# Kernel tuning notes

Hardware: AMD Instinct MI355X
Metric: run time of the kernel (lower is better)

Reference implementation:

```python
import jax, jax.numpy as jnp
import numpy as np

D = 512      # encoder_dim
DI = 1024    # mamba d_inner = expand * d_model
N = 16       # d_state
DTR = 32     # dt_rank = ceil(512/16)
K = 4        # d_conv
B, L = 8, 512


def _ln(x, g, b, eps=1e-5):
    m = jnp.mean(x, -1, keepdims=True)
    v = jnp.mean((x - m) ** 2, -1, keepdims=True)
    return (x - m) / jnp.sqrt(v + eps) * g + b


def _silu(x):
    return x * jax.nn.sigmoid(x)


def _ffn(x, g, b, w1, b1, w2, b2):
    h = _ln(x, g, b)
    h = _silu(h @ w1.T + b1)
    return h @ w2.T + b2


def _dwconv(x, w, pl, pr):
    # x: (B,C,L); w: (C,K) depthwise kernel
    return jax.lax.conv_general_dilated(
        x, w[:, None, :], (1,), [(pl, pr)],
        feature_group_count=x.shape[1], dimension_numbers=('NCH', 'OIH', 'NCH'))


def _mamba(x, win, convw, convb, wx, wdt, bdt, Alog, Dp, wout):
    b = x.shape[0]
    xz = jnp.einsum('bld,ed->ble', x, win)            # (B,L,2*DI)
    xi, z = jnp.split(xz, 2, -1)
    xc = _dwconv(xi.transpose(0, 2, 1), convw, K - 1, 0) + convb[None, :, None]
    xc = _silu(xc).transpose(0, 2, 1)                 # (B,L,DI) causal conv + silu
    xdb = jnp.einsum('bld,ed->ble', xc, wx)           # (B,L,DTR+2N)
    dt, Bm, Cm = xdb[..., :DTR], xdb[..., DTR:DTR + N], xdb[..., DTR + N:]
    dt = jax.nn.softplus(jnp.einsum('blr,dr->bld', dt, wdt) + bdt)
    A = -jnp.exp(Alog)                                # (DI,N)
    dA = jnp.exp(dt[..., None] * A)                   # (B,L,DI,N)
    dBx = dt[..., None] * Bm[:, :, None, :] * xc[..., None]

    def step(h, t):
        dA_t, dBx_t, C_t = t
        h = dA_t * h + dBx_t
        return h, jnp.einsum('bdn,bn->bd', h, C_t)

    h0 = jnp.zeros((b, DI, N), x.dtype)
    _, ys = jax.lax.scan(step, h0, (dA.transpose(1, 0, 2, 3),
                                    dBx.transpose(1, 0, 2, 3),
                                    Cm.transpose(1, 0, 2)))
    y = ys.transpose(1, 0, 2) + Dp * xc
    y = y * _silu(z)
    return jnp.einsum('bld,od->blo', y, wout)


def _bimamba(x, m_win, m_convw, m_convb, m_wx, m_wdt, m_bdt, m_Alog, m_D, m_wout, bi_wo, bi_bo):
    f = _mamba(x, m_win[0], m_convw[0], m_convb[0], m_wx[0], m_wdt[0], m_bdt[0],
               m_Alog[0], m_D[0], m_wout[0])
    r = _mamba(x[:, ::-1], m_win[1], m_convw[1], m_convb[1], m_wx[1], m_wdt[1], m_bdt[1],
               m_Alog[1], m_D[1], m_wout[1])
    cat = jnp.concatenate([f, r[:, ::-1]], -1)
    return cat @ bi_wo.T + bi_bo


def _convmod(x, ln_g, ln_b, pw1_w, pw1_b, dw15, dw31, dw63,
             bn_g, bn_b, bn_m, bn_v, pw2_w, pw2_b):
    h = _ln(x, ln_g, ln_b).transpose(0, 2, 1)          # (B,D,L)
    h = jnp.einsum('bcl,oc->bol', h, pw1_w) + pw1_b[None, :, None]
    a, g = jnp.split(h, 2, 1)
    h = a * jax.nn.sigmoid(g)                          # GLU on channel dim
    outs = [_dwconv(h, w, (w.shape[-1] - 1) // 2, (w.shape[-1] - 1) // 2)
            for w in (dw15, dw31, dw63)]
    out = (outs[0] + outs[1] + outs[2]) / 3.0          # merge_mode='avg'
    out = (out - bn_m[None, :, None]) / jnp.sqrt(bn_v[None, :, None] + 1e-5) \
          * bn_g[None, :, None] + bn_b[None, :, None]
    out = _silu(out)
    out = jnp.einsum('bcl,oc->bol', out, pw2_w) + pw2_b[None, :, None]
    return out.transpose(0, 2, 1)


def setup_inputs() -> dict:
    key = jax.random.key(0)
    ks = iter(jax.random.split(key, 64))
    def w(*shape, s=0.02):
        return jax.random.normal(next(ks), shape, jnp.float32) * s
    inp = {}
    inp['x'] = jax.random.normal(next(ks), (B, L, D), jnp.float32)
    for p in ('ff1', 'ff2'):
        inp[p + '_ln_g'] = jnp.ones((D,), jnp.float32)
        inp[p + '_ln_b'] = jnp.zeros((D,), jnp.float32)
        inp[p + '_w1'] = w(4 * D, D)
        inp[p + '_b1'] = jnp.zeros((4 * D,), jnp.float32)
        inp[p + '_w2'] = w(D, 4 * D)
        inp[p + '_b2'] = jnp.zeros((D,), jnp.float32)
    inp['m_win'] = w(2, 2 * DI, D)
    inp['m_convw'] = w(2, DI, K, s=0.1)
    inp['m_convb'] = jnp.zeros((2, DI), jnp.float32)
    inp['m_wx'] = w(2, DTR + 2 * N, DI)
    inp['m_wdt'] = w(2, DI, DTR, s=0.1)
    inp['m_bdt'] = jnp.full((2, DI), float(np.log(np.expm1(0.01))), jnp.float32)
    inp['m_Alog'] = jnp.log(jnp.tile(jnp.arange(1, N + 1, dtype=jnp.float32), (2, DI, 1)))
    inp['m_D'] = jnp.ones((2, DI), jnp.float32)
    inp['m_wout'] = w(2, D, DI)
    inp['bi_wo'] = w(D, 2 * D)
    inp['bi_bo'] = jnp.zeros((D,), jnp.float32)
    inp['cv_ln_g'] = jnp.ones((D,), jnp.float32)
    inp['cv_ln_b'] = jnp.zeros((D,), jnp.float32)
    inp['cv_pw1_w'] = w(2 * D, D)
    inp['cv_pw1_b'] = jnp.zeros((2 * D,), jnp.float32)
    inp['cv_dw15'] = w(D, 15, s=0.1)
    inp['cv_dw31'] = w(D, 31, s=0.1)
    inp['cv_dw63'] = w(D, 63, s=0.1)
    inp['cv_bn_g'] = jnp.ones((D,), jnp.float32)
    inp['cv_bn_b'] = jnp.zeros((D,), jnp.float32)
    inp['cv_bn_m'] = jnp.zeros((D,), jnp.float32)
    inp['cv_bn_v'] = jnp.ones((D,), jnp.float32)
    inp['cv_pw2_w'] = w(D, D)
    inp['cv_pw2_b'] = jnp.zeros((D,), jnp.float32)
    inp['ln_g'] = jnp.ones((D,), jnp.float32)
    inp['ln_b'] = jnp.zeros((D,), jnp.float32)
    return inp


def reference(x, ff1_ln_g, ff1_ln_b, ff1_w1, ff1_b1, ff1_w2, ff1_b2,
              ff2_ln_g, ff2_ln_b, ff2_w1, ff2_b1, ff2_w2, ff2_b2,
              m_win, m_convw, m_convb, m_wx, m_wdt, m_bdt, m_Alog, m_D, m_wout,
              bi_wo, bi_bo,
              cv_ln_g, cv_ln_b, cv_pw1_w, cv_pw1_b, cv_dw15, cv_dw31, cv_dw63,
              cv_bn_g, cv_bn_b, cv_bn_m, cv_bn_v, cv_pw2_w, cv_pw2_b,
              ln_g, ln_b):
    h = x + 0.5 * _ffn(x, ff1_ln_g, ff1_ln_b, ff1_w1, ff1_b1, ff1_w2, ff1_b2)
    h = h + _bimamba(h, m_win, m_convw, m_convb, m_wx, m_wdt, m_bdt,
                     m_Alog, m_D, m_wout, bi_wo, bi_bo)
    h = h + _convmod(h, cv_ln_g, cv_ln_b, cv_pw1_w, cv_pw1_b, cv_dw15, cv_dw31, cv_dw63,
                     cv_bn_g, cv_bn_b, cv_bn_m, cv_bn_v, cv_pw2_w, cv_pw2_b)
    h = h + 0.5 * _ffn(h, ff2_ln_g, ff2_ln_b, ff2_w1, ff2_b1, ff2_w2, ff2_b2)
    return _ln(h, ln_g, ln_b)
```

## Files before the change

kernel.cpp:

```cpp
#include <hip/hip_runtime.h>
#include <hip/hip_bf16.h>
#include <math.h>

#define LL   512
#define DD   512
#define DII  1024
#define NST  16
#define BB   8
#define MM   4096
#define CHL  32
#define NCH  16
#define MB_  (1024*1024)
#define Q_(n) ((size_t)(n)*262144)

typedef __attribute__((ext_vector_type(8))) short bf16x8;
typedef __attribute__((ext_vector_type(4))) float f32x4;

__device__ __forceinline__ float fast_rcp(float x){ return __builtin_amdgcn_rcpf(x); }
__device__ __forceinline__ float sigmoidf_(float x){ return fast_rcp(1.0f + __expf(-x)); }
__device__ __forceinline__ float siluf_(float x){ return x * sigmoidf_(x); }
__device__ __forceinline__ float softplusf_(float x){
    return fmaxf(x, 0.0f) + __logf(1.0f + __expf(-fabsf(x)));
}

__device__ __forceinline__ short f2bf(float f) {
    union { float f; unsigned u; } v; v.f = f;
    unsigned r = v.u + 0x7fffu + ((v.u >> 16) & 1u);
    return (short)(r >> 16);
}
__device__ __forceinline__ float bf2f(short s) {
    union { unsigned u; float f; } v; v.u = ((unsigned)(unsigned short)s) << 16;
    return v.f;
}
__device__ __forceinline__ bf16x8 pack_bf8(float4 v0, float4 v1) {
    union { bf16x8 v; short e[8]; } pk;
    pk.e[0]=f2bf(v0.x); pk.e[1]=f2bf(v0.y); pk.e[2]=f2bf(v0.z); pk.e[3]=f2bf(v0.w);
    pk.e[4]=f2bf(v1.x); pk.e[5]=f2bf(v1.y); pk.e[6]=f2bf(v1.z); pk.e[7]=f2bf(v1.w);
    return pk.v;
}
__device__ __forceinline__ void gl_lds16(const short* g, short* l) {
    __builtin_amdgcn_global_load_lds(
        (const __attribute__((address_space(1))) void*)g,
        (__attribute__((address_space(3))) void*)l, 16, 0, 0);
}

struct WcvtArgs { const float* s[10]; short* d[10]; int n[10]; };
__global__ void __launch_bounds__(256) wcvt_kernel(WcvtArgs a) {
    const int seg = blockIdx.y;
    const int i = (blockIdx.x*256 + threadIdx.x) * 8;
    if (i >= a.n[seg]) return;
    const float* s = a.s[seg] + i;
    float4 v0 = *(const float4*)s;
    float4 v1 = *(const float4*)(s + 4);
    int di = i;
    if (seg == 8) di = ((i >> 5) << 6) | (i & 31);
    *(bf16x8*)(a.d[seg] + di) = pack_bf8(v0, v1);
}

__global__ void __launch_bounds__(256) woutT_kernel(
    const float* __restrict__ wout, short* __restrict__ outT)
{
    __shared__ float sh[64][65];
    const int o0 = blockIdx.x << 6;
    const int j0 = blockIdx.y << 6;
    const int d  = blockIdx.z;
    const float* in = wout + (size_t)d*512*1024;
    short* out = outT + (size_t)d*1024*512;
    const int t = threadIdx.x;
    const int c4 = (t & 15) << 2;
    const int r  = t >> 4;
    #pragma unroll
    for (int i = 0; i < 4; i++) {
        int orow = r + i*16;
        float4 v = *(const float4*)(in + (size_t)(o0 + orow)*1024 + j0 + c4);
        sh[orow][c4+0]=v.x; sh[orow][c4+1]=v.y; sh[orow][c4+2]=v.z; sh[orow][c4+3]=v.w;
    }
    __syncthreads();
    #pragma unroll
    for (int i = 0; i < 4; i++) {
        int jr = r + i*16;
        short4 o;
        o.x = f2bf(sh[c4+0][jr]); o.y = f2bf(sh[c4+1][jr]);
        o.z = f2bf(sh[c4+2][jr]); o.w = f2bf(sh[c4+3][jr]);
        *(short4*)(out + (size_t)(j0 + jr)*512 + o0 + c4) = o;
    }
}

template<int BN>
__global__ void __launch_bounds__(256) gemm3_kernel(
    const short* __restrict__ A, int lda,
    const short* __restrict__ W, int ldw,
    const float* __restrict__ bias,
    float* __restrict__ outF, short* __restrict__ outB, int ldc,
    int kLen, int kOff, int act, int actLim,
    size_t zA, size_t zW, int zB, size_t zO, int rowsPerW,
    float* __restrict__ partial, size_t pstride, int N)
{
    constexpr int WN = BN / 64;
    constexpr int WM = 4 / WN;
    constexpr int TM = 64 / WM;
    constexpr int FM = TM / 16;
    constexpr int WRW = BN / 32;

    __shared__ short As[2][64*64];
    __shared__ short Ws[2][BN*64];

    const int tid = threadIdx.x, lane = tid & 63, wid = tid >> 6;
    const int z = blockIdx.z;
    A += (size_t)z * zA;
    if (outF) outF += (size_t)z * zO;
    if (outB) outB += (size_t)z * zO;

    int nwg = gridDim.x * gridDim.y;
    int flat = blockIdx.y * gridDim.x + blockIdx.x;
    if (!(nwg & 7)) { int cpx = nwg >> 3; flat = (flat & 7)*cpx + (flat >> 3); }
    const int bx = flat % gridDim.x, by = flat / gridDim.x;

    const int rowBase = by << 6;
    const int colBase = bx * BN;
    const int kBase = z * kOff;

    const int dsel = rowsPerW ? (rowBase / rowsPerW) : z;
    W += (size_t)dsel * zW;
    if (bias) bias += (size_t)dsel * (size_t)zB;

    size_t asrc[2];
    #pragma unroll
    for (int rd = 0; rd < 2; rd++) {
        int id = rd*256 + tid, row = id >> 3, u = id & 7;
        asrc[rd] = (size_t)(rowBase + row)*lda + ((u ^ (row & 7)) << 3);
    }
    size_t wsrc[WRW];
    #pragma unroll
    for (int rd = 0; rd < WRW; rd++) {
        int id = rd*256 + tid, row = id >> 3, u = id & 7;
        wsrc[rd] = (size_t)(colBase + row)*ldw + ((u ^ (row & 7)) << 3);
    }

    const int fr = lane & 15;
    const int swz0 = ((((lane >> 4)    ) ^ (lane & 7)) << 3);
    const int swz1 = ((((lane >> 4) | 4) ^ (lane & 7)) << 3);
    const int wm = (wid / WN) * TM, wn = (wid % WN) * 64;

    f32x4 acc[FM][4] = {};

    auto STAGE = [&](int buf, int k0) {
        #pragma unroll
        for (int rd = 0; rd < 2; rd++)
            gl_lds16(A + asrc[rd] + k0, &As[buf][(rd*256 + tid)*8]);
        #pragma unroll
        for (int rd = 0; rd < WRW; rd++)
            gl_lds16(W + wsrc[rd] + k0, &Ws[buf][(rd*256 + tid)*8]);
    };

    const int nT = kLen >> 6;
    STAGE(0, kBase);
    int cur = 0;
    for (int t = 0; t < nT; ++t) {
        if (t + 1 < nT) {
            STAGE(cur ^ 1, kBase + (t+1)*64);
            asm volatile("s_waitcnt vmcnt(6)" ::: "memory");
        } else {
            asm volatile("s_waitcnt vmcnt(0)" ::: "memory");
        }
        __builtin_amdgcn_sched_barrier(0);
        __builtin_amdgcn_s_barrier();
        __builtin_amdgcn_sched_barrier(0);
        #pragma unroll
        for (int ks = 0; ks < 2; ks++) {
            const int so = ks ? swz1 : swz0;
            bf16x8 af[FM], bfr[4];
            #pragma unroll
            for (int mi = 0; mi < FM; mi++)
                af[mi] = *(const bf16x8*)&As[cur][(wm + mi*16 + fr)*64 + so];
            #pragma unroll
            for (int ni = 0; ni < 4; ni++)
                bfr[ni] = *(const bf16x8*)&Ws[cur][(wn + ni*16 + fr)*64 + so];
            #pragma unroll
            for (int mi = 0; mi < FM; mi++)
                #pragma unroll
                for (int ni = 0; ni < 4; ni++)
                    acc[mi][ni] = __builtin_amdgcn_mfma_f32_16x16x32_bf16(af[mi], bfr[ni], acc[mi][ni], 0, 0, 0);
        }
        __builtin_amdgcn_sched_barrier(0);
        __builtin_amdgcn_s_barrier();
        __builtin_amdgcn_sched_barrier(0);
        cur ^= 1;
    }

    if (partial) {
        float* pp = partial + (size_t)z * pstride;
        #pragma unroll
        for (int mi = 0; mi < FM; mi++)
            #pragma unroll
            for (int r = 0; r < 4; r++) {
                int orow = rowBase + wm + mi*16 + ((lane>>4)<<2) + r;
                #pragma unroll
                for (int ni = 0; ni < 4; ni++)
                    pp[(size_t)orow*N + colBase + wn + ni*16 + fr] = acc[mi][ni][r];
            }
    } else {
        #pragma unroll
        for (int mi = 0; mi < FM; mi++)
            #pragma unroll
            for (int r = 0; r < 4; r++) {
                int orow = rowBase + wm + mi*16 + ((lane>>4)<<2) + r;
                #pragma unroll
                for (int ni = 0; ni < 4; ni++) {
                    int gcol = colBase + wn + ni*16 + fr;
                    float v = acc[mi][ni][r];
                    if (bias) v += bias[gcol];
                    if (gcol < actLim) {
                        if (act == 1) v = siluf_(v);
                        else if (act == 2) v = softplusf_(v);
                    }
                    if (outF) outF[(size_t)orow*ldc + gcol] = v;
                    if (outB) outB[(size_t)orow*ldc + gcol] = f2bf(v);
                }
            }
    }
}

__global__ void __launch_bounds__(256) reduce_kernel(
    const float* __restrict__ part, int S, size_t pstride, int N,
    short* __restrict__ outB, int ldc)
{
    const int i4 = blockIdx.x*256 + threadIdx.x;
    const int row = i4 / (N >> 2);
    const int c4  = (i4 - row*(N >> 2)) << 2;
    float4 s = *(const float4*)(part + (size_t)row*N + c4);
    for (int z = 1; z < S; z++) {
        float4 t = *(const float4*)(part + (size_t)z*pstride + (size_t)row*N + c4);
        s.x += t.x; s.y += t.y; s.z += t.z; s.w += t.w;
    }
    short4 o; o.x=f2bf(s.x); o.y=f2bf(s.y); o.z=f2bf(s.z); o.w=f2bf(s.w);
    *(short4*)(outB + (size_t)row*ldc + c4) = o;
}

__global__ void __launch_bounds__(128) redln_kernel(
    const float* __restrict__ part, int S,
    const float* __restrict__ bias,
    const float* __restrict__ resid, float rscale,
    float* __restrict__ houtF, short* __restrict__ houtB,
    const float* __restrict__ lng, const float* __restrict__ lnb2,
    float* __restrict__ lnoutF, short* __restrict__ lnoutB)
{
    const int row = blockIdx.x;
    const int t = threadIdx.x;
    const size_t pstride = (size_t)MM*512;
    float4 s = ((const float4*)(part + (size_t)row*512))[t];
    for (int z = 1; z < S; z++) {
        float4 v = ((const float4*)(part + z*pstride + (size_t)row*512))[t];
        s.x += v.x; s.y += v.y; s.z += v.z; s.w += v.w;
    }
    if (bias) { float4 b = ((const float4*)bias)[t]; s.x+=b.x; s.y+=b.y; s.z+=b.z; s.w+=b.w; }
    if (resid) {
        float4 r = ((const float4*)(resid + (size_t)row*512))[t];
        s.x = r.x + rscale*s.x; s.y = r.y + rscale*s.y;
        s.z = r.z + rscale*s.z; s.w = r.w + rscale*s.w;
    }
    if (houtF) ((float4*)(houtF + (size_t)row*512))[t] = s;
    if (houtB) {
        short4 o; o.x=f2bf(s.x); o.y=f2bf(s.y); o.z=f2bf(s.z); o.w=f2bf(s.w);
        *(short4*)(houtB + (size_t)row*512 + t*4) = o;
    }
    if (!lng) return;
    float sum = s.x+s.y+s.z+s.w;
    float sq  = s.x*s.x+s.y*s.y+s.z*s.z+s.w*s.w;
    #pragma unroll
    for (int off = 32; off >= 1; off >>= 1) {
        sum += __shfl_down(sum, off);
        sq  += __shfl_down(sq, off);
    }
    __shared__ float sh[4];
    if ((t & 63) == 0) { sh[(t>>6)*2] = sum; sh[(t>>6)*2+1] = sq; }
    __syncthreads();
    float mean = (sh[0]+sh[2]) * (1.0f/512.f);
    float var  = (sh[1]+sh[3]) * (1.0f/512.f) - mean*mean;
    float rstd = rsqrtf(var + 1e-5f);
    float4 gg = ((const float4*)lng)[t];
    float4 bb = ((const float4*)lnb2)[t];
    float4 o;
    o.x = (s.x-mean)*rstd*gg.x + bb.x;
    o.y = (s.y-mean)*rstd*gg.y + bb.y;
    o.z = (s.z-mean)*rstd*gg.z + bb.z;
    o.w = (s.w-mean)*rstd*gg.w + bb.w;
    if (lnoutF) ((float4*)(lnoutF + (size_t)row*512))[t] = o;
    if (lnoutB) {
        short4 ob; ob.x=f2bf(o.x); ob.y=f2bf(o.y); ob.z=f2bf(o.z); ob.w=f2bf(o.w);
        *(short4*)(lnoutB + (size_t)row*512 + t*4) = ob;
    }
}

__global__ void __launch_bounds__(128) ln_kernel(
    const float* __restrict__ x, const float* __restrict__ g,
    const float* __restrict__ bta, short* __restrict__ outB)
{
    const int row = blockIdx.x;
    const int t = threadIdx.x;
    float4 v = ((const float4*)(x + (size_t)row*DD))[t];
    float s = v.x+v.y+v.z+v.w;
    float q = v.x*v.x+v.y*v.y+v.z*v.z+v.w*v.w;
    #pragma unroll
    for (int off = 32; off >= 1; off >>= 1) {
        s += __shfl_down(s, off);
        q += __shfl_down(q, off);
    }
    __shared__ float sh[4];
    if ((t & 63) == 0) { sh[(t>>6)*2] = s; sh[(t>>6)*2+1] = q; }
    __syncthreads();
    float mean = (sh[0]+sh[2]) * (1.0f/DD);
    float var  = (sh[1]+sh[3]) * (1.0f/DD) - mean*mean;
    float rstd = rsqrtf(var + 1e-5f);
    float4 gg = ((const float4*)g)[t];
    float4 bb = ((const float4*)bta)[t];
    short4 ob;
    ob.x = f2bf((v.x-mean)*rstd*gg.x + bb.x);
    ob.y = f2bf((v.y-mean)*rstd*gg.y + bb.y);
    ob.z = f2bf((v.z-mean)*rstd*gg.z + bb.z);
    ob.w = f2bf((v.w-mean)*rstd*gg.w + bb.w);
    *(short4*)(outB + (size_t)row*DD + t*4) = ob;
}

__global__ void __launch_bounds__(256) conv_both_kernel(
    const short* __restrict__ xz_all, const float* __restrict__ cw,
    const float* __restrict__ cb, short* __restrict__ xc_both)
{
    const int gid = blockIdx.x*256 + threadIdx.x;
    const int c4  = (gid & 255) << 2;
    const int row = (gid >> 8) & (MM-1);
    const int dir = gid >> 20;
    const int l   = row & (LL-1);
    const short* base = xz_all + (size_t)(row - l)*4096 + dir*2048 + c4;
    float acc[4];
    #pragma unroll
    for (int j = 0; j < 4; j++) acc[j] = cb[dir*1024 + c4 + j];
    float wt[4][4];
    #pragma unroll
    for (int j = 0; j < 4; j++) {
        float4 w = *(const float4*)(cw + (size_t)dir*4096 + (c4 + j)*4);
        wt[j][0]=w.x; wt[j][1]=w.y; wt[j][2]=w.z; wt[j][3]=w.w;
    }
    #pragma unroll
    for (int t = 0; t < 4; t++) {
        int lt = dir ? (l + 3 - t) : (l - 3 + t);
        if (lt >= 0 && lt < LL) {
            short4 u = *(const short4*)(base + (size_t)lt*4096);
            acc[0] += wt[0][t]*bf2f(u.x);
            acc[1] += wt[1][t]*bf2f(u.y);
            acc[2] += wt[2][t]*bf2f(u.z);
            acc[3] += wt[3][t]*bf2f(u.w);
        }
    }
    short4 o;
    o.x = f2bf(siluf_(acc[0])); o.y = f2bf(siluf_(acc[1]));
    o.z = f2bf(siluf_(acc[2])); o.w = f2bf(siluf_(acc[3]));
    *(short4*)(xc_both + (size_t)dir*MM*1024 + (size_t)row*1024 + c4) = o;
}

__global__ void __launch_bounds__(256) scan_a_kernel(
    const short* __restrict__ dt_bf, const short* __restrict__ xc_both,
    const short* __restrict__ xdb_bf, const float* __restrict__ Alog,
    float* __restrict__ S_dt, float* __restrict__ H)
{
    const int bid = blockIdx.x;
    const int dg  = bid & 3;
    const int c   = (bid >> 2) & (NCH-1);
    const int b   = (bid >> 6) & 7;
    const int dir = bid >> 9;
    const int d   = (dg << 8) + threadIdx.x;

    float Aexp[16];
    #pragma unroll
    for (int n = 0; n < 16; n++) Aexp[n] = -__expf(Alog[dir*16384 + d*16 + n]);
    const float A0 = Aexp[0];
    int fast = 1;
    #pragma unroll
    for (int n = 1; n < 16; n++)
        fast &= (fabsf(Aexp[n] - (float)(n+1)*A0) <= 1e-4f*fabsf(Aexp[n]) + 1e-6f);

    float h[16];
    #pragma unroll
    for (int n = 0; n < 16; n++) h[n] = 0.f;
    float S = 0.f;

    const size_t rbase = (size_t)b*LL + (size_t)c*CHL;
    const short* dtp = dt_bf + ((size_t)dir*MM + rbase)*1024 + d;
    const short* bcp = xdb_bf + ((size_t)dir*MM + rbase)*64 + 32;
    const short* xcp = xc_both + ((size_t)dir*MM + rbase)*1024 + d;

#define SCAN_A_BODY(FASTQ) \
    for (int i = 0; i < CHL; i++) { \
        int lp = dir ? (CHL-1-i) : i; \
        float dtv = bf2f(dtp[(size_t)lp*1024]); \
        float xcv = bf2f(xcp[(size_t)lp*1024]); \
        S += dtv; \
        float co = dtv*xcv; \
        union { bf16x8 v; short e[8]; } b0, b1; \
        b0.v = *(const bf16x8*)(bcp + (size_t)lp*64); \
        b1.v = *(const bf16x8*)(bcp + (size_t)lp*64 + 8); \
        float q[16]; \
        if (FASTQ) { \
            float p = __expf(dtv*A0); float qq = p; \
            _Pragma("unroll") for (int n = 0; n < 16; n++) { q[n] = qq; qq *= p; } \
        } else { \
            _Pragma("unroll") for (int n = 0; n < 16; n++) q[n] = __expf(dtv*Aexp[n]); \
        } \
        _Pragma("unroll") for (int n = 0; n < 16; n++) { \
            float Bv = bf2f(n < 8 ? b0.e[n] : b1.e[n & 7]); \
            h[n] = fmaf(q[n], h[n], co*Bv); \
        } \
    }
    if (fast) { SCAN_A_BODY(1) } else { SCAN_A_BODY(0) }
#undef SCAN_A_BODY

    S_dt[(((size_t)dir*BB + b)*NCH + c)*1024 + d] = S;
    const size_t hb = ((((size_t)dir*BB + b)*NCH + c)*16)*1024 + d;
    #pragma unroll
    for (int n = 0; n < 16; n++) H[hb + (size_t)n*1024] = h[n];
}

__global__ void __launch_bounds__(256) scan_b_kernel(
    const float* __restrict__ S_dt, float* H, const float* __restrict__ Alog)
{
    const int g = blockIdx.x*256 + threadIdx.x;
    const int d = g & 1023;
    const int n = (g >> 10) & 15;
    const int b = (g >> 14) & 7;
    const int dir = g >> 17;
    const float Aexp = -__expf(Alog[dir*16384 + d*16 + n]);
    float h = 0.f;
    for (int ci = 0; ci < NCH; ci++) {
        int c = dir ? (NCH-1-ci) : ci;
        float S = S_dt[(((size_t)dir*BB + b)*NCH + c)*1024 + d];
        size_t i = ((((size_t)dir*BB + b)*NCH + c)*16 + n)*1024 + d;
        float q = __expf(Aexp*S);
        float hn = q*h + H[i];
        H[i] = h;
        h = hn;
    }
}

__global__ void __launch_bounds__(256) scan_c_kernel(
    const short* __restrict__ dt_bf, short* xc_ys,
    const short* __restrict__ xdb_bf, const float* __restrict__ Alog,
    const float* __restrict__ H, const short* __restrict__ xz_all,
    const float* __restrict__ Dp)
{
    const int bid = blockIdx.x;
    const int dg  = bid & 3;
    const int c   = (bid >> 2) & (NCH-1);
    const int b   = (bid >> 6) & 7;
    const int dir = bid >> 9;
    const int d   = (dg << 8) + threadIdx.x;

    float Aexp[16];
    #pragma unroll
    for (int n = 0; n < 16; n++) Aexp[n] = -__expf(Alog[dir*16384 + d*16 + n]);
    const float A0 = Aexp[0];
    int fast = 1;
    #pragma unroll
    for (int n = 1; n < 16; n++)
        fast &= (fabsf(Aexp[n] - (float)(n+1)*A0) <= 1e-4f*fabsf(Aexp[n]) + 1e-6f);
    const float Dpv = Dp[dir*1024 + d];

    float h[16];
    const size_t hb = ((((size_t)dir*BB + b)*NCH + c)*16)*1024 + d;
    #pragma unroll
    for (int n = 0; n < 16; n++) h[n] = H[hb + (size_t)n*1024];

    const size_t rbase = (size_t)b*LL + (size_t)c*CHL;
    const short* dtp = dt_bf + ((size_t)dir*MM + rbase)*1024 + d;
    const short* bcp = xdb_bf + ((size_t)dir*MM + rbase)*64 + 32;
    short*       xcp = xc_ys + ((size_t)dir*MM + rbase)*1024 + d;
    const short* zp  = xz_all + rbase*4096 + dir*2048 + 1024 + d;

#define SCAN_C_BODY(FASTQ) \
    for (int i = 0; i < CHL; i++) { \
        int lp = dir ? (CHL-1-i) : i; \
        float dtv = bf2f(dtp[(size_t)lp*1024]); \
        float xcv = bf2f(xcp[(size_t)lp*1024]); \
        float zv  = bf2f(zp[(size_t)lp*4096]); \
        float co = dtv*xcv; \
        union { bf16x8 v; short e[8]; } b0, b1, c0, c1; \
        b0.v = *(const bf16x8*)(bcp + (size_t)lp*64); \
        b1.v = *(const bf16x8*)(bcp + (size_t)lp*64 + 8); \
        c0.v = *(const bf16x8*)(bcp + (size_t)lp*64 + 16); \
        c1.v = *(const bf16x8*)(bcp + (size_t)lp*64 + 24); \
        float q[16]; \
        if (FASTQ) { \
            float p = __expf(dtv*A0); float qq = p; \
            _Pragma("unroll") for (int n = 0; n < 16; n++) { q[n] = qq; qq *= p; } \
        } else { \
            _Pragma("unroll") for (int n = 0; n < 16; n++) q[n] = __expf(dtv*Aexp[n]); \
        } \
        float y = 0.f; \
        _Pragma("unroll") for (int n = 0; n < 16; n++) { \
            float Bv = bf2f(n < 8 ? b0.e[n] : b1.e[n & 7]); \
            float Cv = bf2f(n < 8 ? c0.e[n] : c1.e[n & 7]); \
            h[n] = fmaf(q[n], h[n], co*Bv); \
            y = fmaf(Cv, h[n], y); \
        } \
        float out = (y + Dpv*xcv) * siluf_(zv); \
        xcp[(size_t)lp*1024] = f2bf(out); \
    }
    if (fast) { SCAN_C_BODY(1) } else { SCAN_C_BODY(0) }
#undef SCAN_C_BODY
}

__global__ void __launch_bounds__(256) glu_transpose_kernel(
    const float* __restrict__ pw1, float* __restrict__ out_t)
{
    __shared__ float sh[64][65];
    const int c0 = blockIdx.x << 6;
    const int l0 = blockIdx.y << 6;
    const int b  = blockIdx.z;
    const int t  = threadIdx.x;
    const int c4 = (t & 15) << 2;
    const int r  = t >> 4;
    #pragma unroll
    for (int i = 0; i < 4; i++) {
        int lrow = r + i*16;
        size_t row = (size_t)(b << 9) + l0 + lrow;
        float4 a = *(const float4*)(pw1 + row*1024 + c0 + c4);
        float4 g = *(const float4*)(pw1 + row*1024 + 512 + c0 + c4);
        sh[lrow][c4+0] = a.x * sigmoidf_(g.x);
        sh[lrow][c4+1] = a.y * sigmoidf_(g.y);
        sh[lrow][c4+2] = a.z * sigmoidf_(g.z);
        sh[lrow][c4+3] = a.w * sigmoidf_(g.w);
    }
    __syncthreads();
    #pragma unroll
    for (int i = 0; i < 4; i++) {
        int crow = r + i*16;
        float4 o;
        o.x = sh[c4+0][crow];
        o.y = sh[c4+1][crow];
        o.z = sh[c4+2][crow];
        o.w = sh[c4+3][crow];
        *(float4*)(out_t + ((size_t)(b << 9) + c0 + crow)*512 + l0 + c4) = o;
    }
}

__global__ void __launch_bounds__(256) multiconv_t_kernel(
    const float* __restrict__ gin_t,
    const float* __restrict__ w15, const float* __restrict__ w31,
    const float* __restrict__ w63,
    const float* __restrict__ bn_g, const float* __restrict__ bn_b,
    const float* __restrict__ bn_m, const float* __restrict__ bn_v,
    float* __restrict__ out_t)
{
    __shared__ float sh[574];
    const int c = blockIdx.x & (DD-1);
    const int b = blockIdx.x >> 9;
    const int t = threadIdx.x;
    const float* rowp = gin_t + ((size_t)(b << 9) + c)*512;
    sh[31 + t]       = rowp[t];
    sh[31 + t + 256] = rowp[t + 256];
    if (t < 31) { sh[t] = 0.f; sh[543 + t] = 0.f; }
    __syncthreads();

    const float bnscale = rsqrtf(bn_v[c] + 1e-5f) * bn_g[c];
    const float bnm = bn_m[c], bnb = bn_b[c];
    float* outp = out_t + ((size_t)(b << 9) + c)*512;
    #pragma unroll
    for (int half = 0; half < 2; half++) {
        int l = t + half*256;
        float s63 = 0.f, s31 = 0.f, s15 = 0.f;
        #pragma unroll
        for (int k = 0; k < 63; k++) s63 += w63[c*63 + k] * sh[l + k];
        #pragma unroll
        for (int k = 0; k < 31; k++) s31 += w31[c*31 + k] * sh[l + 16 + k];
        #pragma unroll
        for (int k = 0; k < 15; k++) s15 += w15[c*15 + k] * sh[l + 24 + k];
        float m = (s15 + s31 + s63) * (1.0f/3.0f);
        m = (m - bnm) * bnscale + bnb;
        outp[l] = siluf_(m);
    }
}

__global__ void __launch_bounds__(256) transpose_bcl_kernel(
    const float* __restrict__ in_t, short* __restrict__ out)
{
    __shared__ float sh[64][65];
    const int l0 = blockIdx.x << 6;
    const int c0 = blockIdx.y << 6;
    const int b  = blockIdx.z;
    const int t  = threadIdx.x;
    const int l4 = (t & 15) << 2;
    const int r  = t >> 4;
    #pragma unroll
    for (int i = 0; i < 4; i++) {
        int crow = r + i*16;
        float4 v = *(const float4*)(in_t + ((size_t)(b << 9) + c0 + crow)*512 + l0 + l4);
        sh[crow][l4+0] = v.x; sh[crow][l4+1] = v.y;
        sh[crow][l4+2] = v.z; sh[crow][l4+3] = v.w;
    }
    __syncthreads();
    #pragma unroll
    for (int i = 0; i < 4; i++) {
        int lrow = r + i*16;
        short4 o;
        o.x = f2bf(sh[l4+0][lrow]);
        o.y = f2bf(sh[l4+1][lrow]);
        o.z = f2bf(sh[l4+2][lrow]);
        o.w = f2bf(sh[l4+3][lrow]);
        *(short4*)(out + ((size_t)(b << 9) + l0 + lrow)*512 + c0 + l4) = o;
    }
}

extern "C" void kernel_launch(void* const* d_in, const int* in_sizes, int n_in,
                              void* d_out, int out_size, void* d_ws, size_t ws_size,
                              hipStream_t stream)
{
    const float* x        = (const float*)d_in[0];
    const float* ff1_ln_g = (const float*)d_in[1];
    const float* ff1_ln_b = (const float*)d_in[2];
    const float* ff1_w1   = (const float*)d_in[3];
    const float* ff1_b1   = (const float*)d_in[4];
    const float* ff1_w2   = (const float*)d_in[5];
    const float* ff1_b2   = (const float*)d_in[6];
    const float* ff2_ln_g = (const float*)d_in[7];
    const float* ff2_ln_b = (const float*)d_in[8];
    const float* ff2_w1   = (const float*)d_in[9];
    const float* ff2_b1   = (const float*)d_in[10];
    const float* ff2_w2   = (const float*)d_in[11];
    const float* ff2_b2   = (const float*)d_in[12];
    const float* m_win    = (const float*)d_in[13];
    const float* m_convw  = (const float*)d_in[14];
    const float* m_convb  = (const float*)d_in[15];
    const float* m_wx     = (const float*)d_in[16];
    const float* m_wdt    = (const float*)d_in[17];
    const float* m_bdt    = (const float*)d_in[18];
    const float* m_Alog   = (const float*)d_in[19];
    const float* m_Dp     = (const float*)d_in[20];
    const float* m_wout   = (const float*)d_in[21];
    const float* bi_wo    = (const float*)d_in[22];
    const float* bi_bo    = (const float*)d_in[23];
    const float* cv_ln_g  = (const float*)d_in[24];
    const float* cv_ln_b  = (const float*)d_in[25];
    const float* cv_pw1_w = (const float*)d_in[26];
    const float* cv_pw1_b = (const float*)d_in[27];
    const float* cv_dw15  = (const float*)d_in[28];
    const float* cv_dw31  = (const float*)d_in[29];
    const float* cv_dw63  = (const float*)d_in[30];
    const float* cv_bn_g  = (const float*)d_in[31];
    const float* cv_bn_b  = (const float*)d_in[32];
    const float* cv_bn_m  = (const float*)d_in[33];
    const float* cv_bn_v  = (const float*)d_in[34];
    const float* cv_pw2_w = (const float*)d_in[35];
    const float* cv_pw2_b = (const float*)d_in[36];
    const float* ln_g     = (const float*)d_in[37];
    const float* ln_b     = (const float*)d_in[38];

    char* wsb = (char*)d_ws;
    float* h        = (float*)(wsb + Q_(0));
    short* h_bf     = (short*)(wsb + Q_(32));
    short* lnb_bf   = (short*)(wsb + Q_(48));
    short* w_ff1w1  = (short*)(wsb + Q_(64));
    short* w_ff1w2  = (short*)(wsb + Q_(72));
    short* w_ff2w1  = (short*)(wsb + Q_(80));
    short* w_ff2w2  = (short*)(wsb + Q_(88));
    short* w_win    = (short*)(wsb + Q_(96));
    short* w_pw1    = (short*)(wsb + Q_(112));
    short* w_pw2    = (short*)(wsb + Q_(116));
    short* w_Wc     = (short*)(wsb + Q_(118));
    short* w_wdtp   = (short*)(wsb + Q_(126));
    short* w_wx     = (short*)(wsb + Q_(127));
    float* part     = (float*)(wsb + Q_(128));
    float* Hbuf     = (float*)(wsb + Q_(128));
    float* S_dt     = (float*)(wsb + Q_(192));
    short* xz_all   = (short*)(wsb + Q_(226));
    short* woutT_ov = (short*)(wsb + Q_(226));
    short* biwo_ov  = (short*)(wsb + Q_(234));
    float* glu_t    = (float*)(wsb + Q_(226));
    short* xc_both  = (short*)(wsb + Q_(290));
    short* hid_bf   = (short*)(wsb + Q_(290));
    short* dt_bf    = (short*)(wsb + Q_(354));
    float* mconv_o  = (float*)(wsb + Q_(354));
    short* xdb_bf   = (short*)(wsb + Q_(418));

    if (ws_size < Q_(422)) return;

    hipMemsetAsync(w_wdtp, 0, (size_t)2*1024*64*2, stream);
    WcvtArgs wa;
    wa.s[0]=ff1_w1;   wa.d[0]=w_ff1w1; wa.n[0]=1048576;
    wa.s[1]=ff1_w2;   wa.d[1]=w_ff1w2; wa.n[1]=1048576;
    wa.s[2]=ff2_w1;   wa.d[2]=w_ff2w1; wa.n[2]=1048576;
    wa.s[3]=ff2_w2;   wa.d[3]=w_ff2w2; wa.n[3]=1048576;
    wa.s[4]=m_win;    wa.d[4]=w_win;   wa.n[4]=2097152;
    wa.s[5]=bi_wo;    wa.d[5]=biwo_ov; wa.n[5]=524288;
    wa.s[6]=cv_pw1_w; wa.d[6]=w_pw1;   wa.n[6]=524288;
    wa.s[7]=cv_pw2_w; wa.d[7]=w_pw2;   wa.n[7]=262144;
    wa.s[8]=m_wdt;    wa.d[8]=w_wdtp;  wa.n[8]=65536;
    wa.s[9]=m_wx;     wa.d[9]=w_wx;    wa.n[9]=131072;
    wcvt_kernel<<<dim3(1024,10), 256, 0, stream>>>(wa);
    woutT_kernel<<<dim3(8,16,2), 256, 0, stream>>>(m_wout, woutT_ov);

    auto G = [&](const short* A, int lda, const short* W, int ldw,
                 const float* bias, float* oF, short* oB, int ldc,
                 int M, int N, int nz, int kLen, int kOff,
                 size_t zA, size_t zW, int zB, size_t zO, int rowsPerW,
                 int act, int actLim, float* prt) {
        dim3 g(N/128, M/64, nz);
        gemm3_kernel<128><<<g, 256, 0, stream>>>(A, lda, W, ldw, bias, oF, oB, ldc,
            kLen, kOff, act, actLim, zA, zW, zB, zO, rowsPerW,
            prt, (size_t)M*N, N);
    };

    G(biwo_ov, 1024, woutT_ov, 512, nullptr, nullptr, w_Wc, 1024,
      512, 1024, 2, 512, 0, 512, 524288, 0, 524288, 0, 0, 0, nullptr);

    ln_kernel<<<MM, 128, 0, stream>>>(x, ff1_ln_g, ff1_ln_b, lnb_bf);
    G(lnb_bf, 512, w_ff1w1, 512, ff1_b1, nullptr, hid_bf, 2048,
      MM, 2048, 1, 512, 0, 0, 0, 0, 0, 0, 1, 2048, nullptr);
    G(hid_bf, 2048, w_ff1w2, 2048, nullptr, nullptr, nullptr, 0,
      MM, 512, 2, 1024, 1024, 0, 0, 0, 0, 0, 0, 0, part);
    redln_kernel<<<MM, 128, 0, stream>>>(part, 2, ff1_b2, x, 0.5f,
        h, h_bf, nullptr, nullptr, nullptr, nullptr);

    G(h_bf, 512, w_win, 512, nullptr, nullptr, xz_all, 4096,
      MM, 4096, 1, 512, 0, 0, 0, 0, 0, 0, 0, 0, nullptr);
    conv_both_kernel<<<8192, 256, 0, stream>>>(xz_all, m_convw, m_convb, xc_both);
    {
        dim3 g(1, 128, 4);
        gemm3_kernel<64><<<g, 256, 0, stream>>>(xc_both, 1024, w_wx, 1024,
            nullptr, nullptr, nullptr, 0, 256, 256, 0, 0,
            0, 65536, 0, 0, 4096, part, (size_t)8192*64, 64);
    }
    reduce_kernel<<<512, 256, 0, stream>>>(part, 4, (size_t)8192*64, 64, xdb_bf, 64);
    G(xdb_bf, 64, w_wdtp, 64, m_bdt, nullptr, dt_bf, 1024,
      8192, 1024, 1, 64, 0, 0, 65536, 1024, 0, 4096, 2, 1024, nullptr);
    scan_a_kernel<<<1024, 256, 0, stream>>>(dt_bf, xc_both, xdb_bf, m_Alog, S_dt, Hbuf);
    scan_b_kernel<<<1024, 256, 0, stream>>>(S_dt, Hbuf, m_Alog);
    scan_c_kernel<<<1024, 256, 0, stream>>>(dt_bf, xc_both, xdb_bf, m_Alog, Hbuf,
                                            xz_all, m_Dp);
    G(xc_both, 1024, w_Wc, 1024, nullptr, nullptr, nullptr, 0,
      MM, 512, 2, 1024, 0, (size_t)MM*1024, 524288, 0, 0, 0, 0, 0, part);
    redln_kernel<<<MM, 128, 0, stream>>>(part, 2, bi_bo, h, 1.0f,
        h, nullptr, cv_ln_g, cv_ln_b, nullptr, lnb_bf);

    G(lnb_bf, 512, w_pw1, 512, cv_pw1_b, part, nullptr, 1024,
      MM, 1024, 1, 512, 0, 0, 0, 0, 0, 0, 0, 0, nullptr);
    glu_transpose_kernel<<<dim3(8,8,8), 256, 0, stream>>>(part, glu_t);
    multiconv_t_kernel<<<BB*DD, 256, 0, stream>>>(glu_t,
        cv_dw15, cv_dw31, cv_dw63, cv_bn_g, cv_bn_b, cv_bn_m, cv_bn_v, mconv_o);
    transpose_bcl_kernel<<<dim3(8,8,8), 256, 0, stream>>>(mconv_o, lnb_bf);
    G(lnb_bf, 512, w_pw2, 512, nullptr, nullptr, nullptr, 0,
      MM, 512, 2, 256, 256, 0, 0, 0, 0, 0, 0, 0, part);
    redln_kernel<<<MM, 128, 0, stream>>>(part, 2, cv_pw2_b, h, 1.0f,
        h, nullptr, ff2_ln_g, ff2_ln_b, nullptr, lnb_bf);

    G(lnb_bf, 512, w_ff2w1, 512, ff2_b1, nullptr, hid_bf, 2048,
      MM, 2048, 1, 512, 0, 0, 0, 0, 0, 0, 1, 2048, nullptr);
    G(hid_bf, 2048, w_ff2w2, 2048, nullptr, nullptr, nullptr, 0,
      MM, 512, 2, 1024, 1024, 0, 0, 0, 0, 0, 0, 0, part);
    redln_kernel<<<MM, 128, 0, stream>>>(part, 2, ff2_b2, h, 0.5f,
        nullptr, nullptr, ln_g, ln_b, (float*)d_out, nullptr);
}
```

Before: 392.8 us.

## Add 128x256-tile double-buffered MFMA GEMM for wide-N projections

Adds a new 512-thread GEMM kernel with 128x256 output tiles, XOR-swizzled LDS, direct global-to-LDS loads, double buffering and an XCD-aware block remap. It replaces the generic 64x128 GEMM for the two FFN up-projections and the Mamba input projection, which are the large-N, K=512 matmuls. The aim is more data reuse per tile and better memory/compute overlap. The trade-off is higher LDS use (96KB), fewer blocks, and an epilogue that writes scalar bf16 with a per-element bias check.

```diff
diff --git a/kernel.cpp b/kernel.cpp
--- a/kernel.cpp
+++ b/kernel.cpp
@@ -84,6 +84,105 @@
         o.z = f2bf(sh[c4+2][jr]); o.w = f2bf(sh[c4+3][jr]);
         *(short4*)(out + (size_t)(j0 + jr)*512 + o0 + c4) = o;
     }
+}
+
+__global__ void __launch_bounds__(512) gemm9_kernel(
+    const short* __restrict__ A, int lda,
+    const short* __restrict__ W, int ldw,
+    const float* __restrict__ bias,
+    short* __restrict__ outB, int ldc,
+    int kLen, int act)
+{
+    __shared__ short As[2][128*64];
+    __shared__ short Ws[2][256*64];
+
+    const int tid = threadIdx.x, lane = tid & 63, wid = tid >> 6;
+
+    int nwg = gridDim.x * gridDim.y;
+    int flat = blockIdx.y * gridDim.x + blockIdx.x;
+    if (!(nwg & 7)) { int cpx = nwg >> 3; flat = (flat & 7)*cpx + (flat >> 3); }
+    const int bx = flat % gridDim.x, by = flat / gridDim.x;
+    const int rowBase = by << 7;
+    const int colBase = bx << 8;
+
+    size_t asrc[2];
+    #pragma unroll
+    for (int rd = 0; rd < 2; rd++) {
+        int id = rd*512 + tid, row = id >> 3, u = id & 7;
+        asrc[rd] = (size_t)(rowBase + row)*lda + ((u ^ (row & 7)) << 3);
+    }
+    size_t wsrc[4];
+    #pragma unroll
+    for (int rd = 0; rd < 4; rd++) {
+        int id = rd*512 + tid, row = id >> 3, u = id & 7;
+        wsrc[rd] = (size_t)(colBase + row)*ldw + ((u ^ (row & 7)) << 3);
+    }
+
+    const int fr = lane & 15;
+    const int swz0 = ((((lane >> 4)    ) ^ (lane & 7)) << 3);
+    const int swz1 = ((((lane >> 4) | 4) ^ (lane & 7)) << 3);
+    const int wm = (wid >> 2) * 64, wn = (wid & 3) * 64;
+
+    f32x4 acc[4][4] = {};
+
+    auto STAGE = [&](int buf, int k0) {
+        #pragma unroll
+        for (int rd = 0; rd < 2; rd++)
+            gl_lds16(A + asrc[rd] + k0, &As[buf][(rd*512 + tid)*8]);
+        #pragma unroll
+        for (int rd = 0; rd < 4; rd++)
+            gl_lds16(W + wsrc[rd] + k0, &Ws[buf][(rd*512 + tid)*8]);
+    };
+
+    const int nT = kLen >> 6;
+    STAGE(0, 0);
+    int cur = 0;
+    for (int t = 0; t < nT; ++t) {
+        if (t + 1 < nT) {
+            STAGE(cur ^ 1, (t+1)*64);
+            asm volatile("s_waitcnt vmcnt(6)" ::: "memory");
+        } else {
+            asm volatile("s_waitcnt vmcnt(0)" ::: "memory");
+        }
+        __builtin_amdgcn_sched_barrier(0);
+        __builtin_amdgcn_s_barrier();
+        __builtin_amdgcn_sched_barrier(0);
+        #pragma unroll
+        for (int ks = 0; ks < 2; ks++) {
+            const int so = ks ? swz1 : swz0;
+            bf16x8 af[4], bfr[4];
+            #pragma unroll
+            for (int mi = 0; mi < 4; mi++)
+                af[mi] = *(const bf16x8*)&As[cur][(wm + mi*16 + fr)*64 + so];
+            #pragma unroll
+            for (int ni = 0; ni < 4; ni++)
+                bfr[ni] = *(const bf16x8*)&Ws[cur][(wn + ni*16 + fr)*64 + so];
+            #pragma unroll
+            for (int mi = 0; mi < 4; mi++)
+                #pragma unroll
+                for (int ni = 0; ni < 4; ni++)
+                    acc[mi][ni] = __builtin_amdgcn_mfma_f32_16x16x32_bf16(af[mi], bfr[ni], acc[mi][ni], 0, 0, 0);
+        }
+        __builtin_amdgcn_sched_barrier(0);
+        __builtin_amdgcn_s_barrier();
+        __builtin_amdgcn_sched_barrier(0);
+        cur ^= 1;
+    }
+
+    #pragma unroll
+    for (int mi = 0; mi < 4; mi++)
+        #pragma unroll
+        for (int r = 0; r < 4; r++) {
+            int orow = rowBase + wm + mi*16 + ((lane>>4)<<2) + r;
+            #pragma unroll
+            for (int ni = 0; ni < 4; ni++) {
+                int gcol = colBase + wn + ni*16 + fr;
+                float v = acc[mi][ni][r];
+                if (bias) v += bias[gcol];
+                if (act == 1) v = siluf_(v);
+                outB[(size_t)orow*ldc + gcol] = f2bf(v);
+            }
+        }
 }
 
 template<int BN>
@@ -712,15 +811,15 @@
       512, 1024, 2, 512, 0, 512, 524288, 0, 524288, 0, 0, 0, nullptr);
 
     ln_kernel<<<MM, 128, 0, stream>>>(x, ff1_ln_g, ff1_ln_b, lnb_bf);
-    G(lnb_bf, 512, w_ff1w1, 512, ff1_b1, nullptr, hid_bf, 2048,
-      MM, 2048, 1, 512, 0, 0, 0, 0, 0, 0, 1, 2048, nullptr);
+    gemm9_kernel<<<dim3(8, 32), 512, 0, stream>>>(lnb_bf, 512, w_ff1w1, 512,
+        ff1_b1, hid_bf, 2048, 512, 1);
     G(hid_bf, 2048, w_ff1w2, 2048, nullptr, nullptr, nullptr, 0,
       MM, 512, 2, 1024, 1024, 0, 0, 0, 0, 0, 0, 0, part);
     redln_kernel<<<MM, 128, 0, stream>>>(part, 2, ff1_b2, x, 0.5f,
         h, h_bf, nullptr, nullptr, nullptr, nullptr);
 
-    G(h_bf, 512, w_win, 512, nullptr, nullptr, xz_all, 4096,
-      MM, 4096, 1, 512, 0, 0, 0, 0, 0, 0, 0, 0, nullptr);
+    gemm9_kernel<<<dim3(16, 32), 512, 0, stream>>>(h_bf, 512, w_win, 512,
+        nullptr, xz_all, 4096, 512, 0);
     conv_both_kernel<<<8192, 256, 0, stream>>>(xz_all, m_convw, m_convb, xc_both);
     {
         dim3 g(1, 128, 4);
@@ -751,8 +850,8 @@
     redln_kernel<<<MM, 128, 0, stream>>>(part, 2, cv_pw2_b, h, 1.0f,
         h, nullptr, ff2_ln_g, ff2_ln_b, nullptr, lnb_bf);
 
-    G(lnb_bf, 512, w_ff2w1, 512, ff2_b1, nullptr, hid_bf, 2048,
-      MM, 2048, 1, 512, 0, 0, 0, 0, 0, 0, 1, 2048, nullptr);
+    gemm9_kernel<<<dim3(8, 32), 512, 0, stream>>>(lnb_bf, 512, w_ff2w1, 512,
+        ff2_b1, hid_bf, 2048, 512, 1);
     G(hid_bf, 2048, w_ff2w2, 2048, nullptr, nullptr, nullptr, 0,
       MM, 512, 2, 1024, 1024, 0, 0, 0, 0, 0, 0, 0, part);
     redln_kernel<<<MM, 128, 0, stream>>>(part, 2, ff2_b2, h, 0.5f,
```

New measurement: 377.1 us. -4.0%, faster.
